# Kernel optimization log

Measured on AMD Instinct MI355X. Metric: run time of the kernel, lower is better.

## Reference

```python
import jax, jax.numpy as jnp
import numpy as np

N_LAYERS = 6
N_HEADS = 16
D_MODEL = 1024
D_HEAD = D_MODEL // N_HEADS
D_FF = 4096
VOCAB = 32000
MAX_LEN = 1024
B, T = 2, 1024
NEG = -1e9
EPS = 1e-5


def layernorm(x, s, b):
    mu = jnp.mean(x, axis=-1, keepdims=True)
    var = jnp.mean(jnp.square(x - mu), axis=-1, keepdims=True)
    return (x - mu) * jax.lax.rsqrt(var + EPS) * s + b


def setup_inputs() -> dict:
    key = jax.random.key(0)
    ks = jax.random.split(key, 8)
    s = 0.02
    return {
        "idx": jax.random.randint(ks[0], (B, T), 0, VOCAB),
        "tok_emb": jax.random.normal(ks[1], (VOCAB, D_MODEL), jnp.float32) * s,
        "pos_emb": jax.random.normal(ks[2], (MAX_LEN, D_MODEL), jnp.float32) * s,
        "ln1_s": jnp.ones((N_LAYERS, D_MODEL), jnp.float32),
        "ln1_b": jnp.zeros((N_LAYERS, D_MODEL), jnp.float32),
        "qkv_w": jax.random.normal(ks[3], (N_LAYERS, D_MODEL, 3 * D_MODEL), jnp.float32) * s,
        "qkv_b": jnp.zeros((N_LAYERS, 3 * D_MODEL), jnp.float32),
        "out_w": jax.random.normal(ks[4], (N_LAYERS, D_MODEL, D_MODEL), jnp.float32) * s,
        "out_b": jnp.zeros((N_LAYERS, D_MODEL), jnp.float32),
        "ln2_s": jnp.ones((N_LAYERS, D_MODEL), jnp.float32),
        "ln2_b": jnp.zeros((N_LAYERS, D_MODEL), jnp.float32),
        "mlp_w1": jax.random.normal(ks[5], (N_LAYERS, D_MODEL, D_FF), jnp.float32) * s,
        "mlp_b1": jnp.zeros((N_LAYERS, D_FF), jnp.float32),
        "mlp_w2": jax.random.normal(ks[6], (N_LAYERS, D_FF, D_MODEL), jnp.float32) * s,
        "mlp_b2": jnp.zeros((N_LAYERS, D_MODEL), jnp.float32),
        "lnf_s": jnp.ones((D_MODEL,), jnp.float32),
        "lnf_b": jnp.zeros((D_MODEL,), jnp.float32),
        "head_w": jax.random.normal(ks[7], (D_MODEL, VOCAB), jnp.float32) * s,
    }


def reference(idx, tok_emb, pos_emb, ln1_s, ln1_b, qkv_w, qkv_b, out_w, out_b,
              ln2_s, ln2_b, mlp_w1, mlp_b1, mlp_w2, mlp_b2, lnf_s, lnf_b, head_w):
    b, t = idx.shape
    x = tok_emb[idx] + pos_emb[:t]  # [B,T,D]
    causal = jnp.tril(jnp.ones((t, t), dtype=bool))
    scale = 1.0 / np.sqrt(D_HEAD)
    for l in range(N_LAYERS):
        h = layernorm(x, ln1_s[l], ln1_b[l])
        qkv = h @ qkv_w[l] + qkv_b[l]  # [B,T,3D]
        q, k, v = jnp.split(qkv, 3, axis=-1)
        q = q.reshape(b, t, N_HEADS, D_HEAD).transpose(0, 2, 1, 3)
        k = k.reshape(b, t, N_HEADS, D_HEAD).transpose(0, 2, 1, 3)
        v = v.reshape(b, t, N_HEADS, D_HEAD).transpose(0, 2, 1, 3)
        att = jnp.einsum('bhqd,bhkd->bhqk', q, k) * scale
        att = jnp.where(causal, att, NEG)
        att = jax.nn.softmax(att, axis=-1)
        y = jnp.einsum('bhqk,bhkd->bhqd', att, v)
        y = y.transpose(0, 2, 1, 3).reshape(b, t, D_MODEL)
        x = x + (y @ out_w[l] + out_b[l])
        h = layernorm(x, ln2_s[l], ln2_b[l])
        m = jax.nn.gelu(h @ mlp_w1[l] + mlp_b1[l], approximate=False) @ mlp_w2[l] + mlp_b2[l]
        x = x + m
    x = layernorm(x, lnf_s, lnf_b)
    logits = x @ head_w  # [B,T,V]
    return logits
```

## Files before the change

kernel.cpp:

```cpp
#include <hip/hip_runtime.h>


#define T_SEQ 1024
#define NTOK  2048
#define DM    1024
#define DFF   4096
#define NH    16
#define DH    64
#define NL    6
#define VOCAB 32000

typedef short sx8 __attribute__((ext_vector_type(8)));
typedef float fx4 __attribute__((ext_vector_type(4)));
typedef unsigned short usx4 __attribute__((ext_vector_type(4)));
typedef unsigned int   uix4 __attribute__((ext_vector_type(4)));

__device__ __forceinline__ unsigned short f2bf(float f) {
  union { float f; unsigned u; } c; c.f = f;
  unsigned r = c.u + 0x7FFFu + ((c.u >> 16) & 1u);
  return (unsigned short)(r >> 16);
}
__device__ __forceinline__ float bf2f(unsigned short u) {
  union { unsigned u; float f; } c; c.u = ((unsigned)u) << 16;
  return c.f;
}

__device__ __forceinline__ void gload_lds16(const unsigned short* g, unsigned short* l) {
  __builtin_amdgcn_global_load_lds(
      (const __attribute__((address_space(1))) unsigned int*)g,
      (__attribute__((address_space(3))) unsigned int*)l, 16, 0, 0);
}

__device__ __forceinline__ int xcd_swizzle(int orig, int nwg) {
  int q = nwg >> 3, r = nwg & 7;
  int xcd = orig & 7, idx = orig >> 3;
  int base = (xcd < r) ? xcd * (q + 1) : r * (q + 1) + (xcd - r) * q;
  return base + idx;
}

__global__ __launch_bounds__(256) void k_embed(const int* __restrict__ idx,
                                               const float* __restrict__ tok,
                                               const float* __restrict__ pos,
                                               float* __restrict__ x) {
  int token = blockIdx.x;
  int t = token & (T_SEQ - 1);
  int id = idx[token];
  int c = threadIdx.x * 4;
  float4 tv = *(const float4*)&tok[(size_t)id * DM + c];
  float4 pv = *(const float4*)&pos[(size_t)t * DM + c];
  float4 r;
  r.x = tv.x + pv.x; r.y = tv.y + pv.y; r.z = tv.z + pv.z; r.w = tv.w + pv.w;
  *(float4*)&x[(size_t)token * DM + c] = r;
}

__global__ __launch_bounds__(256) void k_ln(const float* __restrict__ x,
                                            const float* __restrict__ g,
                                            const float* __restrict__ b,
                                            unsigned short* __restrict__ h) {
  int row = blockIdx.x;
  int tid = threadIdx.x;
  float4 v = *(const float4*)&x[(size_t)row * DM + tid * 4];
  float s = v.x + v.y + v.z + v.w;
  float q = v.x * v.x + v.y * v.y + v.z * v.z + v.w * v.w;
  for (int off = 32; off > 0; off >>= 1) {
    s += __shfl_down(s, off);
    q += __shfl_down(q, off);
  }
  __shared__ float red[8];
  int wid = tid >> 6, lane = tid & 63;
  if (lane == 0) { red[wid] = s; red[4 + wid] = q; }
  __syncthreads();
  s = red[0] + red[1] + red[2] + red[3];
  q = red[4] + red[5] + red[6] + red[7];
  float mu = s * (1.0f / DM);
  float var = q * (1.0f / DM) - mu * mu;
  float rstd = rsqrtf(var + 1e-5f);
  float4 gg = *(const float4*)&g[tid * 4];
  float4 bb = *(const float4*)&b[tid * 4];
  usx4 o;
  o[0] = f2bf((v.x - mu) * rstd * gg.x + bb.x);
  o[1] = f2bf((v.y - mu) * rstd * gg.y + bb.y);
  o[2] = f2bf((v.z - mu) * rstd * gg.z + bb.z);
  o[3] = f2bf((v.w - mu) * rstd * gg.w + bb.w);
  *(usx4*)&h[(size_t)row * DM + tid * 4] = o;
}

__global__ __launch_bounds__(256) void k_reduce_ln(const unsigned short* __restrict__ part,
                                                   float* __restrict__ x,
                                                   const float* __restrict__ g,
                                                   const float* __restrict__ b,
                                                   unsigned short* __restrict__ h) {
  int row = blockIdx.x;
  int tid = threadIdx.x;
  int c = tid * 4;
  float4 v = *(const float4*)&x[(size_t)row * DM + c];
#pragma unroll
  for (int s4 = 0; s4 < 4; ++s4) {
    usx4 p = *(const usx4*)&part[((size_t)s4 * NTOK + row) * DM + c];
    v.x += bf2f(p[0]); v.y += bf2f(p[1]); v.z += bf2f(p[2]); v.w += bf2f(p[3]);
  }
  *(float4*)&x[(size_t)row * DM + c] = v;
  float s = v.x + v.y + v.z + v.w;
  float q = v.x * v.x + v.y * v.y + v.z * v.z + v.w * v.w;
  for (int off = 32; off > 0; off >>= 1) {
    s += __shfl_down(s, off);
    q += __shfl_down(q, off);
  }
  __shared__ float red[8];
  int wid = tid >> 6, lane = tid & 63;
  if (lane == 0) { red[wid] = s; red[4 + wid] = q; }
  __syncthreads();
  s = red[0] + red[1] + red[2] + red[3];
  q = red[4] + red[5] + red[6] + red[7];
  float mu = s * (1.0f / DM);
  float var = q * (1.0f / DM) - mu * mu;
  float rstd = rsqrtf(var + 1e-5f);
  float4 gg = *(const float4*)&g[c];
  float4 bb = *(const float4*)&b[c];
  usx4 o;
  o[0] = f2bf((v.x - mu) * rstd * gg.x + bb.x);
  o[1] = f2bf((v.y - mu) * rstd * gg.y + bb.y);
  o[2] = f2bf((v.z - mu) * rstd * gg.z + bb.z);
  o[3] = f2bf((v.w - mu) * rstd * gg.w + bb.w);
  *(usx4*)&h[(size_t)row * DM + c] = o;
}

__global__ __launch_bounds__(256) void k_wtrans(const float* __restrict__ W,
                                                unsigned short* __restrict__ WT,
                                                int K, int N) {
  __shared__ float t[64][68];
  int k0 = blockIdx.x * 64, n0 = blockIdx.y * 64;
  int tid = threadIdx.x;
#pragma unroll
  for (int i = 0; i < 4; ++i) {
    int chunk = i * 256 + tid;
    int r = chunk >> 4, c = (chunk & 15) << 2;
    float4 v = *(const float4*)&W[(size_t)(k0 + r) * N + n0 + c];
    t[r][c] = v.x; t[r][c + 1] = v.y; t[r][c + 2] = v.z; t[r][c + 3] = v.w;
  }
  __syncthreads();
#pragma unroll
  for (int i = 0; i < 4; ++i) {
    int chunk = i * 256 + tid;
    int n = chunk >> 4, c = (chunk & 15) << 2;
    usx4 o;
    o[0] = f2bf(t[c][n]);
    o[1] = f2bf(t[c + 1][n]);
    o[2] = f2bf(t[c + 2][n]);
    o[3] = f2bf(t[c + 3][n]);
    *(usx4*)&WT[(size_t)(n0 + n) * K + k0 + c] = o;
  }
}

template <int EPI>
__global__ __launch_bounds__(256) void k_gemm(const unsigned short* __restrict__ A,
                                              const unsigned short* __restrict__ BT,
                                              const float* __restrict__ bias,
                                              unsigned short* __restrict__ part,
                                              unsigned short* __restrict__ outb,
                                              float* __restrict__ outf,
                                              int N, int K, int NT, int KS) {
  __shared__ unsigned short As[2][128 * 64];
  __shared__ unsigned short Bs[2][128 * 64];
  int tid = threadIdx.x;
  int wid = tid >> 6, lane = tid & 63;
  int lr = lane & 15, lg = lane >> 4;

  int id = xcd_swizzle(blockIdx.x, gridDim.x);
  int mt = id & 15;
  int rest = id >> 4;
  int nt = rest % NT;
  int ks = rest / NT;
  int m0 = mt * 128, n0 = nt * 128;
  int Kslice = K / KS;
  int kbeg = ks * Kslice;
  int nk = Kslice >> 6;

  int wm = (wid >> 1) * 64, wn = (wid & 1) * 64;

  fx4 acc[4][4] = {};

#define GSTAGE(buf, kt)                                                         \
  {                                                                             \
    _Pragma("unroll")                                                           \
    for (int i = 0; i < 4; ++i) {                                               \
      int chunk = i * 256 + tid;                                                \
      int r = chunk >> 3, slot = chunk & 7;                                     \
      int c = ((slot ^ (r & 7)) << 3);                                          \
      gload_lds16(&A[(size_t)(m0 + r) * K + (kt) + c], &As[buf][chunk << 3]);   \
      gload_lds16(&BT[(size_t)(n0 + r) * K + (kt) + c], &Bs[buf][chunk << 3]);  \
    }                                                                           \
  }

  GSTAGE(0, kbeg);
  for (int ik = 0; ik < nk; ++ik) {
    int cur = ik & 1;
    if (ik + 1 < nk) {
      GSTAGE(cur ^ 1, kbeg + (ik + 1) * 64);
      asm volatile("s_waitcnt vmcnt(8)" ::: "memory");
    } else {
      asm volatile("s_waitcnt vmcnt(0)" ::: "memory");
    }
    __builtin_amdgcn_sched_barrier(0);
    __builtin_amdgcn_s_barrier();
    __builtin_amdgcn_sched_barrier(0);
#pragma unroll
    for (int kk = 0; kk < 2; ++kk) {
      int slotz = (kk * 4 + lg) ^ (lr & 7);
      sx8 fa[4], fb[4];
#pragma unroll
      for (int mi = 0; mi < 4; ++mi)
        fa[mi] = *(const sx8*)&As[cur][(wm + mi * 16 + lr) * 64 + slotz * 8];
#pragma unroll
      for (int ni = 0; ni < 4; ++ni)
        fb[ni] = *(const sx8*)&Bs[cur][(wn + ni * 16 + lr) * 64 + slotz * 8];
#pragma unroll
      for (int mi = 0; mi < 4; ++mi)
#pragma unroll
        for (int ni = 0; ni < 4; ++ni)
          acc[mi][ni] = __builtin_amdgcn_mfma_f32_16x16x32_bf16(fb[ni], fa[mi], acc[mi][ni], 0, 0, 0);
    }
    asm volatile("s_waitcnt lgkmcnt(0)" ::: "memory");
    __builtin_amdgcn_sched_barrier(0);
    __builtin_amdgcn_s_barrier();
  }
#undef GSTAGE

#pragma unroll
  for (int ni = 0; ni < 4; ++ni) {
    int col0 = n0 + wn + ni * 16 + lg * 4;
    float4 bv = {0.f, 0.f, 0.f, 0.f};
    if (bias && ks == 0) bv = *(const float4*)&bias[col0];
#pragma unroll
    for (int mi = 0; mi < 4; ++mi) {
      int row = m0 + wm + mi * 16 + lr;
      float v0 = acc[mi][ni][0] + bv.x;
      float v1 = acc[mi][ni][1] + bv.y;
      float v2 = acc[mi][ni][2] + bv.z;
      float v3 = acc[mi][ni][3] + bv.w;
      if constexpr (EPI == 0) {
        int bb = row >> 10, tt = row & 1023;
        if (col0 < 2048) {
          int which = col0 >> 10;
          int hc = col0 & 1023;
          usx4 o = {f2bf(v0), f2bf(v1), f2bf(v2), f2bf(v3)};
          *(usx4*)&outb[(size_t)which * NTOK * DM +
                        (((size_t)bb * NH + (hc >> 6)) * T_SEQ + tt) * DH + (hc & 63)] = o;
        } else {
          int dc = col0 - 2048;
          unsigned short* vt = outb + (size_t)2 * NTOK * DM;
          size_t base = (((size_t)bb * NH + (dc >> 6)) * DH + (dc & 63)) * T_SEQ + tt;
          vt[base] = f2bf(v0);
          vt[base + T_SEQ] = f2bf(v1);
          vt[base + 2 * T_SEQ] = f2bf(v2);
          vt[base + 3 * T_SEQ] = f2bf(v3);
        }
      } else if constexpr (EPI == 1) {
        usx4 o;
        o[0] = f2bf(0.5f * v0 * (1.0f + erff(v0 * 0.70710678f)));
        o[1] = f2bf(0.5f * v1 * (1.0f + erff(v1 * 0.70710678f)));
        o[2] = f2bf(0.5f * v2 * (1.0f + erff(v2 * 0.70710678f)));
        o[3] = f2bf(0.5f * v3 * (1.0f + erff(v3 * 0.70710678f)));
        *(usx4*)&outb[(size_t)row * N + col0] = o;
      } else {
        usx4 o = {f2bf(v0), f2bf(v1), f2bf(v2), f2bf(v3)};
        *(usx4*)&part[((size_t)ks * NTOK + row) * DM + col0] = o;
      }
    }
  }
}

#define LDSUB(buf, ab, kk) (lds + (((buf) * 2 + (ab)) * 2 + (kk)) * 8192)

__device__ __forceinline__ void stage_half(const unsigned short* g, int rowstride,
                                           unsigned short* ldsbase, int tid, int k0) {
#pragma unroll
  for (int r = 0; r < 2; ++r) {
    int chunk = r * 512 + tid;
    int row = chunk >> 2, slot = chunk & 3;
    gload_lds16(g + (size_t)row * rowstride + k0 + ((slot ^ ((row >> 1) & 3)) << 3),
                ldsbase + (chunk << 3));
  }
}

__global__ __launch_bounds__(512, 2) void k_gemm256(const unsigned short* __restrict__ A,
                                                    const unsigned short* __restrict__ BT,
                                                    float* __restrict__ outf,
                                                    int N, int K) {
  __shared__ unsigned short lds[8 * 8192];
  int tid = threadIdx.x;
  int wid = tid >> 6, lane = tid & 63;
  int lr = lane & 15, lg = lane >> 4;
  int wm2 = wid >> 2, wn4 = wid & 3;
  int id = xcd_swizzle(blockIdx.x, gridDim.x);
  int mt = id & 7, nt = id >> 3;
  int m0 = mt * 256, n0 = nt * 256;
  const unsigned short* Ab = A + (size_t)m0 * K;
  const unsigned short* Bb = BT + (size_t)n0 * K;
  int NIT = K >> 7;
  int swz = (lg ^ ((lr >> 1) & 3)) << 3;
  float* obase = outf + (size_t)(m0 + wm2 * 128 + lr) * N + n0 + wn4 * 64 + lg * 4;

  fx4 acc[8][4] = {};

  stage_half(Ab, K, LDSUB(0, 0, 0), tid, 0);
  stage_half(Bb, K, LDSUB(0, 1, 0), tid, 0);
  stage_half(Ab, K, LDSUB(0, 0, 1), tid, 32);
  stage_half(Bb, K, LDSUB(0, 1, 1), tid, 32);
  stage_half(Ab, K, LDSUB(1, 0, 0), tid, 64);
  stage_half(Bb, K, LDSUB(1, 1, 0), tid, 64);
  stage_half(Ab, K, LDSUB(1, 0, 1), tid, 96);
  asm volatile("s_waitcnt vmcnt(6)" ::: "memory");
  __builtin_amdgcn_s_barrier();

#define PHASE(BUF, KK, NHH, LOADA, STG, VMW)                                         \
  {                                                                                  \
    if (LOADA) {                                                                     \
      const unsigned short* sA = LDSUB(BUF, 0, KK);                                  \
      _Pragma("unroll")                                                              \
      for (int mi = 0; mi < 8; ++mi)                                                 \
        fa[mi] = *(const sx8*)&sA[(wm2 * 128 + mi * 16 + lr) * 32 + swz];            \
    }                                                                                \
    {                                                                                \
      const unsigned short* sB = LDSUB(BUF, 1, KK);                                  \
      _Pragma("unroll")                                                              \
      for (int j = 0; j < 2; ++j)                                                    \
        fb[j] = *(const sx8*)&sB[(wn4 * 64 + (NHH) * 32 + j * 16 + lr) * 32 + swz];  \
    }                                                                                \
    STG;                                                                             \
    VMW;                                                                             \
    __builtin_amdgcn_sched_barrier(0);                                               \
    __builtin_amdgcn_s_barrier();                                                    \
    asm volatile("s_waitcnt lgkmcnt(0)" ::: "memory");                               \
    __builtin_amdgcn_sched_barrier(0);                                               \
    __builtin_amdgcn_s_setprio(1);                                                   \
    _Pragma("unroll")                                                                \
    for (int mi = 0; mi < 8; ++mi) {                                                 \
      acc[mi][(NHH) * 2 + 0] = __builtin_amdgcn_mfma_f32_16x16x32_bf16(              \
          fb[0], fa[mi], acc[mi][(NHH) * 2 + 0], 0, 0, 0);                           \
      acc[mi][(NHH) * 2 + 1] = __builtin_amdgcn_mfma_f32_16x16x32_bf16(              \
          fb[1], fa[mi], acc[mi][(NHH) * 2 + 1], 0, 0, 0);                           \
    }                                                                                \
    __builtin_amdgcn_s_setprio(0);                                                   \
    __builtin_amdgcn_sched_barrier(0);                                               \
    __builtin_amdgcn_s_barrier();                                                    \
  }

  for (int it = 0; it < NIT; ++it) {
    bool st = (it < NIT - 1);
    bool last = (it == NIT - 1);
    int t1k = (2 * it + 1) * 64;
    int t2k = (2 * it + 2) * 64;
    int t3k = (2 * it + 3) * 64;
    sx8 fa[8], fb[2];

    PHASE(0, 0, 0, true,
          { stage_half(Bb, K, LDSUB(1, 1, 1), tid, t1k + 32); }, {});
    PHASE(0, 0, 1, false,
          { if (st) stage_half(Ab, K, LDSUB(0, 0, 0), tid, t2k); }, {});
    PHASE(0, 1, 0, true,
          { if (st) stage_half(Bb, K, LDSUB(0, 1, 0), tid, t2k); }, {});
    PHASE(0, 1, 1, false,
          { if (st) stage_half(Ab, K, LDSUB(0, 0, 1), tid, t2k + 32); },
          { if (last) { asm volatile("s_waitcnt vmcnt(0)" ::: "memory"); }
            else      { asm volatile("s_waitcnt vmcnt(6)" ::: "memory"); } });
    PHASE(1, 0, 0, true,
          { if (st) stage_half(Bb, K, LDSUB(0, 1, 1), tid, t2k + 32); }, {});
    PHASE(1, 0, 1, false,
          { if (st) stage_half(Ab, K, LDSUB(1, 0, 0), tid, t3k); }, {});
    PHASE(1, 1, 0, true,
          { if (st) stage_half(Bb, K, LDSUB(1, 1, 0), tid, t3k); }, {});
    if (last) {
#pragma unroll
      for (int mi = 0; mi < 8; ++mi) {
        *(float4*)(obase + (size_t)mi * 16 * N) =
            (float4){acc[mi][0][0], acc[mi][0][1], acc[mi][0][2], acc[mi][0][3]};
        *(float4*)(obase + (size_t)mi * 16 * N + 16) =
            (float4){acc[mi][1][0], acc[mi][1][1], acc[mi][1][2], acc[mi][1][3]};
      }
    }
    PHASE(1, 1, 1, false,
          { if (st) stage_half(Ab, K, LDSUB(1, 0, 1), tid, t3k + 32); },
          { if (!last) { asm volatile("s_waitcnt vmcnt(6)" ::: "memory"); } });
  }
#undef PHASE

#pragma unroll
  for (int mi = 0; mi < 8; ++mi) {
    *(float4*)(obase + (size_t)mi * 16 * N + 32) =
        (float4){acc[mi][2][0], acc[mi][2][1], acc[mi][2][2], acc[mi][2][3]};
    *(float4*)(obase + (size_t)mi * 16 * N + 48) =
        (float4){acc[mi][3][0], acc[mi][3][1], acc[mi][3][2], acc[mi][3][3]};
  }
}

__global__ __launch_bounds__(256) void k_attn(const unsigned short* __restrict__ gq,
                                              const unsigned short* __restrict__ gk,
                                              const unsigned short* __restrict__ gvt,
                                              unsigned short* __restrict__ y) {
  __shared__ unsigned short Ks[128 * 64];
  __shared__ unsigned short Vt[64 * 128];
  __shared__ unsigned short Pw[4][16 * 136];
  int id = xcd_swizzle(blockIdx.x, gridDim.x);
  int bh = id >> 4, qt = 15 - (id & 15);
  int tid = threadIdx.x, wid = tid >> 6, lane = tid & 63;
  int lr = lane & 15, lg = lane >> 4;
  int q0 = qt * 64 + wid * 16;
  int qg = q0 + lr;
  const float SCL = 0.125f * 1.44269504f;

  sx8 qf[2];
  {
    const unsigned short* qp = gq + ((size_t)bh * T_SEQ + qg) * DH + lg * 8;
    qf[0] = *(const sx8*)qp;
    qf[1] = *(const sx8*)(qp + 32);
  }

  fx4 yacc[4] = {};
  float mrun = -1e30f, lrun = 0.f;

  int jmax = qt >> 1;
  for (int j = 0; j <= jmax; ++j) {
    int kt0 = j * 128;
    __syncthreads();
#pragma unroll
    for (int i = 0; i < 4; ++i) {
      int chunk = i * 256 + tid;
      {
        int r = chunk >> 3, s = chunk & 7;
        gload_lds16(&gk[((size_t)bh * T_SEQ + kt0 + r) * DH + ((s ^ (r & 7)) << 3)],
                    &Ks[chunk << 3]);
      }
      {
        int r = chunk >> 4, s = chunk & 15;
        gload_lds16(&gvt[((size_t)bh * DH + r) * T_SEQ + kt0 + ((s ^ (r & 15)) << 3)],
                    &Vt[chunk << 3]);
      }
    }
    __syncthreads();

    fx4 st[8] = {};
#pragma unroll
    for (int kk = 0; kk < 2; ++kk) {
      int slotz = (kk * 4 + lg) ^ (lr & 7);
#pragma unroll
      for (int mi = 0; mi < 8; ++mi) {
        sx8 kb = *(const sx8*)&Ks[(mi * 16 + lr) * 64 + slotz * 8];
        st[mi] = __builtin_amdgcn_mfma_f32_16x16x32_bf16(kb, qf[kk], st[mi], 0, 0, 0);
      }
    }

    float pvv[8][4];
    float pmax = -1e30f;
    bool lastj = (j == jmax);
#pragma unroll
    for (int mi = 0; mi < 8; ++mi)
#pragma unroll
      for (int rg = 0; rg < 4; ++rg) {
        float val = st[mi][rg] * SCL;
        if (lastj && (kt0 + mi * 16 + lg * 4 + rg) > qg) val = -1e30f;
        pvv[mi][rg] = val;
        pmax = fmaxf(pmax, val);
      }
    pmax = fmaxf(pmax, __shfl_xor(pmax, 16));
    pmax = fmaxf(pmax, __shfl_xor(pmax, 32));
    if (!__all(pmax <= mrun + 11.5f)) {
      float mnew = fmaxf(mrun, pmax);
      float sc = exp2f(mrun - mnew);
      lrun *= sc;
#pragma unroll
      for (int dt = 0; dt < 4; ++dt)
#pragma unroll
        for (int rg = 0; rg < 4; ++rg) yacc[dt][rg] *= sc;
      mrun = mnew;
    }
    float ps = 0.f;
#pragma unroll
    for (int mi = 0; mi < 8; ++mi)
#pragma unroll
      for (int rg = 0; rg < 4; ++rg) {
        float e = exp2f(pvv[mi][rg] - mrun);
        pvv[mi][rg] = e;
        ps += e;
      }
    ps += __shfl_xor(ps, 16);
    ps += __shfl_xor(ps, 32);
    lrun += ps;

#pragma unroll
    for (int mi = 0; mi < 8; ++mi)
#pragma unroll
      for (int rp = 0; rp < 2; ++rp) {
        unsigned pk = (unsigned)f2bf(pvv[mi][rp * 2]) |
                      ((unsigned)f2bf(pvv[mi][rp * 2 + 1]) << 16);
        *(unsigned*)&Pw[wid][lr * 136 + mi * 16 + lg * 4 + rp * 2] = pk;
      }

#pragma unroll
    for (int kk = 0; kk < 4; ++kk) {
      sx8 pa = *(const sx8*)&Pw[wid][lr * 136 + kk * 32 + lg * 8];
      int slotz = (kk * 4 + lg) ^ lr;
#pragma unroll
      for (int dt = 0; dt < 4; ++dt) {
        sx8 vb = *(const sx8*)&Vt[(dt * 16 + lr) * 128 + slotz * 8];
        yacc[dt] = __builtin_amdgcn_mfma_f32_16x16x32_bf16(vb, pa, yacc[dt], 0, 0, 0);
      }
    }
  }

  float inv = 1.0f / lrun;
  int tok = (bh >> 4) * T_SEQ + qg;
  int colbase = (bh & 15) * DH;
#pragma unroll
  for (int dt = 0; dt < 4; ++dt) {
    usx4 o;
#pragma unroll
    for (int rg = 0; rg < 4; ++rg) o[rg] = f2bf(yacc[dt][rg] * inv);
    *(usx4*)&y[(size_t)tok * DM + colbase + dt * 16 + lg * 4] = o;
  }
}

extern "C" void kernel_launch(void* const* d_in, const int* in_sizes, int n_in,
                              void* d_out, int out_size, void* d_ws, size_t ws_size,
                              hipStream_t stream) {
  (void)in_sizes; (void)n_in; (void)out_size; (void)ws_size;
  const int*   idx     = (const int*)d_in[0];
  const float* tok_emb = (const float*)d_in[1];
  const float* pos_emb = (const float*)d_in[2];
  const float* ln1_s   = (const float*)d_in[3];
  const float* ln1_b   = (const float*)d_in[4];
  const float* qkv_w   = (const float*)d_in[5];
  const float* qkv_b   = (const float*)d_in[6];
  const float* out_w   = (const float*)d_in[7];
  const float* out_b   = (const float*)d_in[8];
  const float* ln2_s   = (const float*)d_in[9];
  const float* ln2_b   = (const float*)d_in[10];
  const float* mlp_w1  = (const float*)d_in[11];
  const float* mlp_b1  = (const float*)d_in[12];
  const float* mlp_w2  = (const float*)d_in[13];
  const float* mlp_b2  = (const float*)d_in[14];
  const float* lnf_s   = (const float*)d_in[15];
  const float* lnf_b   = (const float*)d_in[16];
  const float* head_w  = (const float*)d_in[17];

  char* p = (char*)d_ws;
  float* x          = (float*)p;          p += (size_t)NTOK * DM * 4;
  unsigned short* h = (unsigned short*)p; p += (size_t)NTOK * DM * 2;
  unsigned short* qkvb = (unsigned short*)p; p += (size_t)3 * NTOK * DM * 2;
  unsigned short* yb = (unsigned short*)p; p += (size_t)NTOK * DM * 2;
  unsigned short* m1 = (unsigned short*)p; p += (size_t)NTOK * DFF * 2;
  unsigned short* wt = (unsigned short*)p;
  unsigned short* part = (unsigned short*)(p + 32 * 1024 * 1024);

  dim3 blk(256);

  k_embed<<<NTOK, blk, 0, stream>>>(idx, tok_emb, pos_emb, x);
  k_ln<<<NTOK, blk, 0, stream>>>(x, ln1_s, ln1_b, h);

  for (int l = 0; l < NL; ++l) {
    k_wtrans<<<dim3(DM / 64, 3 * DM / 64), blk, 0, stream>>>(qkv_w + (size_t)l * DM * 3 * DM, wt, DM, 3 * DM);
    k_gemm<0><<<16 * 24, blk, 0, stream>>>(h, wt, qkv_b + l * 3 * DM,
                                           nullptr, qkvb, nullptr, 3 * DM, DM, 24, 1);
    k_attn<<<512, blk, 0, stream>>>(qkvb, qkvb + (size_t)NTOK * DM,
                                    qkvb + (size_t)2 * NTOK * DM, yb);
    k_wtrans<<<dim3(DM / 64, DM / 64), blk, 0, stream>>>(out_w + (size_t)l * DM * DM, wt, DM, DM);
    k_gemm<2><<<16 * 8 * 4, blk, 0, stream>>>(yb, wt, out_b + l * DM,
                                              part, nullptr, nullptr, DM, DM, 8, 4);
    k_reduce_ln<<<NTOK, blk, 0, stream>>>(part, x, ln2_s + l * DM, ln2_b + l * DM, h);
    k_wtrans<<<dim3(DM / 64, DFF / 64), blk, 0, stream>>>(mlp_w1 + (size_t)l * DM * DFF, wt, DM, DFF);
    k_gemm<1><<<16 * 32, blk, 0, stream>>>(h, wt, mlp_b1 + l * DFF,
                                           nullptr, m1, nullptr, DFF, DM, 32, 1);
    k_wtrans<<<dim3(DFF / 64, DM / 64), blk, 0, stream>>>(mlp_w2 + (size_t)l * DFF * DM, wt, DFF, DM);
    k_gemm<2><<<16 * 8 * 4, blk, 0, stream>>>(m1, wt, mlp_b2 + l * DM,
                                              part, nullptr, nullptr, DM, DFF, 8, 4);
    if (l < NL - 1)
      k_reduce_ln<<<NTOK, blk, 0, stream>>>(part, x, ln1_s + (l + 1) * DM, ln1_b + (l + 1) * DM, h);
    else
      k_reduce_ln<<<NTOK, blk, 0, stream>>>(part, x, lnf_s, lnf_b, h);
  }

  k_wtrans<<<dim3(DM / 64, VOCAB / 64), blk, 0, stream>>>(head_w, wt, DM, VOCAB);
  k_gemm256<<<1000, 512, 0, stream>>>(h, wt, (float*)d_out, VOCAB, DM);
}
```

Before: 1.160 ms.

## Batch per-layer weight transposes, fuse embed+LN, use packed bf16 conversions

Combines the four per-layer weight transpose launches into one larger launch that writes into separate buffers, and fuses the embedding with the first layernorm. Replaces the software bf16 rounding with the hardware v_cvt_pk_bf16_f32 instruction across all epilogues. Splits the attention causal-mask loop so only the diagonal tile evaluates the mask. The aim is fewer launches, better occupancy for the transpose, and cheaper conversion arithmetic, at the cost of needing more workspace for the transposed weights, which must not overlap the partial-sum buffer.

```diff
diff --git a/kernel.cpp b/kernel.cpp
--- a/kernel.cpp
+++ b/kernel.cpp
@@ -24,6 +24,11 @@
   union { unsigned u; float f; } c; c.u = ((unsigned)u) << 16;
   return c.f;
 }
+__device__ __forceinline__ unsigned cvt_pk_bf16(float lo, float hi) {
+  unsigned r;
+  asm("v_cvt_pk_bf16_f32 %0, %1, %2" : "=v"(r) : "v"(lo), "v"(hi));
+  return r;
+}
 
 __device__ __forceinline__ void gload_lds16(const unsigned short* g, unsigned short* l) {
   __builtin_amdgcn_global_load_lds(
@@ -38,68 +43,23 @@
   return base + idx;
 }
 
-__global__ __launch_bounds__(256) void k_embed(const int* __restrict__ idx,
-                                               const float* __restrict__ tok,
-                                               const float* __restrict__ pos,
-                                               float* __restrict__ x) {
+__global__ __launch_bounds__(256) void k_embed_ln(const int* __restrict__ idx,
+                                                  const float* __restrict__ tok,
+                                                  const float* __restrict__ pos,
+                                                  const float* __restrict__ g,
+                                                  const float* __restrict__ b,
+                                                  float* __restrict__ x,
+                                                  unsigned short* __restrict__ h) {
   int token = blockIdx.x;
   int t = token & (T_SEQ - 1);
   int id = idx[token];
-  int c = threadIdx.x * 4;
+  int tid = threadIdx.x;
+  int c = tid * 4;
   float4 tv = *(const float4*)&tok[(size_t)id * DM + c];
   float4 pv = *(const float4*)&pos[(size_t)t * DM + c];
-  float4 r;
-  r.x = tv.x + pv.x; r.y = tv.y + pv.y; r.z = tv.z + pv.z; r.w = tv.w + pv.w;
-  *(float4*)&x[(size_t)token * DM + c] = r;
-}
-
-__global__ __launch_bounds__(256) void k_ln(const float* __restrict__ x,
-                                            const float* __restrict__ g,
-                                            const float* __restrict__ b,
-                                            unsigned short* __restrict__ h) {
-  int row = blockIdx.x;
-  int tid = threadIdx.x;
-  float4 v = *(const float4*)&x[(size_t)row * DM + tid * 4];
-  float s = v.x + v.y + v.z + v.w;
-  float q = v.x * v.x + v.y * v.y + v.z * v.z + v.w * v.w;
-  for (int off = 32; off > 0; off >>= 1) {
-    s += __shfl_down(s, off);
-    q += __shfl_down(q, off);
-  }
-  __shared__ float red[8];
-  int wid = tid >> 6, lane = tid & 63;
-  if (lane == 0) { red[wid] = s; red[4 + wid] = q; }
-  __syncthreads();
-  s = red[0] + red[1] + red[2] + red[3];
-  q = red[4] + red[5] + red[6] + red[7];
-  float mu = s * (1.0f / DM);
-  float var = q * (1.0f / DM) - mu * mu;
-  float rstd = rsqrtf(var + 1e-5f);
-  float4 gg = *(const float4*)&g[tid * 4];
-  float4 bb = *(const float4*)&b[tid * 4];
-  usx4 o;
-  o[0] = f2bf((v.x - mu) * rstd * gg.x + bb.x);
-  o[1] = f2bf((v.y - mu) * rstd * gg.y + bb.y);
-  o[2] = f2bf((v.z - mu) * rstd * gg.z + bb.z);
-  o[3] = f2bf((v.w - mu) * rstd * gg.w + bb.w);
-  *(usx4*)&h[(size_t)row * DM + tid * 4] = o;
-}
-
-__global__ __launch_bounds__(256) void k_reduce_ln(const unsigned short* __restrict__ part,
-                                                   float* __restrict__ x,
-                                                   const float* __restrict__ g,
-                                                   const float* __restrict__ b,
-                                                   unsigned short* __restrict__ h) {
-  int row = blockIdx.x;
-  int tid = threadIdx.x;
-  int c = tid * 4;
-  float4 v = *(const float4*)&x[(size_t)row * DM + c];
-#pragma unroll
-  for (int s4 = 0; s4 < 4; ++s4) {
-    usx4 p = *(const usx4*)&part[((size_t)s4 * NTOK + row) * DM + c];
-    v.x += bf2f(p[0]); v.y += bf2f(p[1]); v.z += bf2f(p[2]); v.w += bf2f(p[3]);
-  }
-  *(float4*)&x[(size_t)row * DM + c] = v;
+  float4 v;
+  v.x = tv.x + pv.x; v.y = tv.y + pv.y; v.z = tv.z + pv.z; v.w = tv.w + pv.w;
+  *(float4*)&x[(size_t)token * DM + c] = v;
   float s = v.x + v.y + v.z + v.w;
   float q = v.x * v.x + v.y * v.y + v.z * v.z + v.w * v.w;
   for (int off = 32; off > 0; off >>= 1) {
@@ -117,20 +77,54 @@
   float rstd = rsqrtf(var + 1e-5f);
   float4 gg = *(const float4*)&g[c];
   float4 bb = *(const float4*)&b[c];
-  usx4 o;
-  o[0] = f2bf((v.x - mu) * rstd * gg.x + bb.x);
-  o[1] = f2bf((v.y - mu) * rstd * gg.y + bb.y);
-  o[2] = f2bf((v.z - mu) * rstd * gg.z + bb.z);
-  o[3] = f2bf((v.w - mu) * rstd * gg.w + bb.w);
-  *(usx4*)&h[(size_t)row * DM + c] = o;
-}
-
-__global__ __launch_bounds__(256) void k_wtrans(const float* __restrict__ W,
-                                                unsigned short* __restrict__ WT,
-                                                int K, int N) {
+  uint2 o;
+  o.x = cvt_pk_bf16((v.x - mu) * rstd * gg.x + bb.x, (v.y - mu) * rstd * gg.y + bb.y);
+  o.y = cvt_pk_bf16((v.z - mu) * rstd * gg.z + bb.z, (v.w - mu) * rstd * gg.w + bb.w);
+  *(uint2*)&h[(size_t)token * DM + c] = o;
+}
+
+__global__ __launch_bounds__(256) void k_reduce_ln(const unsigned short* __restrict__ part,
+                                                   float* __restrict__ x,
+                                                   const float* __restrict__ g,
+                                                   const float* __restrict__ b,
+                                                   unsigned short* __restrict__ h) {
+  int row = blockIdx.x;
+  int tid = threadIdx.x;
+  int c = tid * 4;
+  float4 v = *(const float4*)&x[(size_t)row * DM + c];
+#pragma unroll
+  for (int s4 = 0; s4 < 4; ++s4) {
+    usx4 p = *(const usx4*)&part[((size_t)s4 * NTOK + row) * DM + c];
+    v.x += bf2f(p[0]); v.y += bf2f(p[1]); v.z += bf2f(p[2]); v.w += bf2f(p[3]);
+  }
+  *(float4*)&x[(size_t)row * DM + c] = v;
+  float s = v.x + v.y + v.z + v.w;
+  float q = v.x * v.x + v.y * v.y + v.z * v.z + v.w * v.w;
+  for (int off = 32; off > 0; off >>= 1) {
+    s += __shfl_down(s, off);
+    q += __shfl_down(q, off);
+  }
+  __shared__ float red[8];
+  int wid = tid >> 6, lane = tid & 63;
+  if (lane == 0) { red[wid] = s; red[4 + wid] = q; }
+  __syncthreads();
+  s = red[0] + red[1] + red[2] + red[3];
+  q = red[4] + red[5] + red[6] + red[7];
+  float mu = s * (1.0f / DM);
+  float var = q * (1.0f / DM) - mu * mu;
+  float rstd = rsqrtf(var + 1e-5f);
+  float4 gg = *(const float4*)&g[c];
+  float4 bb = *(const float4*)&b[c];
+  uint2 o;
+  o.x = cvt_pk_bf16((v.x - mu) * rstd * gg.x + bb.x, (v.y - mu) * rstd * gg.y + bb.y);
+  o.y = cvt_pk_bf16((v.z - mu) * rstd * gg.z + bb.z, (v.w - mu) * rstd * gg.w + bb.w);
+  *(uint2*)&h[(size_t)row * DM + c] = o;
+}
+
+__device__ __forceinline__ void wtrans_body(const float* __restrict__ W,
+                                            unsigned short* __restrict__ WT,
+                                            int K, int N, int k0, int n0, int tid) {
   __shared__ float t[64][68];
-  int k0 = blockIdx.x * 64, n0 = blockIdx.y * 64;
-  int tid = threadIdx.x;
 #pragma unroll
   for (int i = 0; i < 4; ++i) {
     int chunk = i * 256 + tid;
@@ -143,13 +137,35 @@
   for (int i = 0; i < 4; ++i) {
     int chunk = i * 256 + tid;
     int n = chunk >> 4, c = (chunk & 15) << 2;
-    usx4 o;
-    o[0] = f2bf(t[c][n]);
-    o[1] = f2bf(t[c + 1][n]);
-    o[2] = f2bf(t[c + 2][n]);
-    o[3] = f2bf(t[c + 3][n]);
-    *(usx4*)&WT[(size_t)(n0 + n) * K + k0 + c] = o;
-  }
+    uint2 o;
+    o.x = cvt_pk_bf16(t[c][n], t[c + 1][n]);
+    o.y = cvt_pk_bf16(t[c + 2][n], t[c + 3][n]);
+    *(uint2*)&WT[(size_t)(n0 + n) * K + k0 + c] = o;
+  }
+}
+
+__global__ __launch_bounds__(256) void k_wtrans(const float* __restrict__ W,
+                                                unsigned short* __restrict__ WT,
+                                                int K, int N) {
+  wtrans_body(W, WT, K, N, blockIdx.x * 64, blockIdx.y * 64, threadIdx.x);
+}
+
+__global__ __launch_bounds__(256) void k_wtrans4(const float* __restrict__ W0,
+                                                 const float* __restrict__ W1,
+                                                 const float* __restrict__ W2,
+                                                 const float* __restrict__ W3,
+                                                 unsigned short* __restrict__ T0,
+                                                 unsigned short* __restrict__ T1,
+                                                 unsigned short* __restrict__ T2,
+                                                 unsigned short* __restrict__ T3) {
+  int id = blockIdx.x;
+  const float* W; unsigned short* WT; int K, N, lid;
+  if (id < 768)       { W = W0; WT = T0; K = 1024; N = 3072; lid = id; }
+  else if (id < 1024) { W = W1; WT = T1; K = 1024; N = 1024; lid = id - 768; }
+  else if (id < 2048) { W = W2; WT = T2; K = 1024; N = 4096; lid = id - 1024; }
+  else                { W = W3; WT = T3; K = 4096; N = 1024; lid = id - 2048; }
+  int kb = K >> 6;
+  wtrans_body(W, WT, K, N, (lid % kb) * 64, (lid / kb) * 64, threadIdx.x);
 }
 
 template <int EPI>
@@ -243,9 +259,9 @@
         if (col0 < 2048) {
           int which = col0 >> 10;
           int hc = col0 & 1023;
-          usx4 o = {f2bf(v0), f2bf(v1), f2bf(v2), f2bf(v3)};
-          *(usx4*)&outb[(size_t)which * NTOK * DM +
-                        (((size_t)bb * NH + (hc >> 6)) * T_SEQ + tt) * DH + (hc & 63)] = o;
+          uint2 o = {cvt_pk_bf16(v0, v1), cvt_pk_bf16(v2, v3)};
+          *(uint2*)&outb[(size_t)which * NTOK * DM +
+                         (((size_t)bb * NH + (hc >> 6)) * T_SEQ + tt) * DH + (hc & 63)] = o;
         } else {
           int dc = col0 - 2048;
           unsigned short* vt = outb + (size_t)2 * NTOK * DM;
@@ -256,15 +272,15 @@
           vt[base + 3 * T_SEQ] = f2bf(v3);
         }
       } else if constexpr (EPI == 1) {
-        usx4 o;
-        o[0] = f2bf(0.5f * v0 * (1.0f + erff(v0 * 0.70710678f)));
-        o[1] = f2bf(0.5f * v1 * (1.0f + erff(v1 * 0.70710678f)));
-        o[2] = f2bf(0.5f * v2 * (1.0f + erff(v2 * 0.70710678f)));
-        o[3] = f2bf(0.5f * v3 * (1.0f + erff(v3 * 0.70710678f)));
-        *(usx4*)&outb[(size_t)row * N + col0] = o;
+        float g0 = 0.5f * v0 * (1.0f + erff(v0 * 0.70710678f));
+        float g1 = 0.5f * v1 * (1.0f + erff(v1 * 0.70710678f));
+        float g2 = 0.5f * v2 * (1.0f + erff(v2 * 0.70710678f));
+        float g3 = 0.5f * v3 * (1.0f + erff(v3 * 0.70710678f));
+        uint2 o = {cvt_pk_bf16(g0, g1), cvt_pk_bf16(g2, g3)};
+        *(uint2*)&outb[(size_t)row * N + col0] = o;
       } else {
-        usx4 o = {f2bf(v0), f2bf(v1), f2bf(v2), f2bf(v3)};
-        *(usx4*)&part[((size_t)ks * NTOK + row) * DM + col0] = o;
+        uint2 o = {cvt_pk_bf16(v0, v1), cvt_pk_bf16(v2, v3)};
+        *(uint2*)&part[((size_t)ks * NTOK + row) * DM + col0] = o;
       }
     }
   }
@@ -452,16 +468,26 @@
 
     float pvv[8][4];
     float pmax = -1e30f;
-    bool lastj = (j == jmax);
-#pragma unroll
-    for (int mi = 0; mi < 8; ++mi)
-#pragma unroll
-      for (int rg = 0; rg < 4; ++rg) {
-        float val = st[mi][rg] * SCL;
-        if (lastj && (kt0 + mi * 16 + lg * 4 + rg) > qg) val = -1e30f;
-        pvv[mi][rg] = val;
-        pmax = fmaxf(pmax, val);
-      }
+    if (j < jmax) {
+#pragma unroll
+      for (int mi = 0; mi < 8; ++mi)
+#pragma unroll
+        for (int rg = 0; rg < 4; ++rg) {
+          float val = st[mi][rg] * SCL;
+          pvv[mi][rg] = val;
+          pmax = fmaxf(pmax, val);
+        }
+    } else {
+#pragma unroll
+      for (int mi = 0; mi < 8; ++mi)
+#pragma unroll
+        for (int rg = 0; rg < 4; ++rg) {
+          float val = st[mi][rg] * SCL;
+          if ((kt0 + mi * 16 + lg * 4 + rg) > qg) val = -1e30f;
+          pvv[mi][rg] = val;
+          pmax = fmaxf(pmax, val);
+        }
+    }
     pmax = fmaxf(pmax, __shfl_xor(pmax, 16));
     pmax = fmaxf(pmax, __shfl_xor(pmax, 32));
     if (!__all(pmax <= mrun + 11.5f)) {
@@ -491,8 +517,7 @@
     for (int mi = 0; mi < 8; ++mi)
 #pragma unroll
       for (int rp = 0; rp < 2; ++rp) {
-        unsigned pk = (unsigned)f2bf(pvv[mi][rp * 2]) |
-                      ((unsigned)f2bf(pvv[mi][rp * 2 + 1]) << 16);
+        unsigned pk = cvt_pk_bf16(pvv[mi][rp * 2], pvv[mi][rp * 2 + 1]);
         *(unsigned*)&Pw[wid][lr * 136 + mi * 16 + lg * 4 + rp * 2] = pk;
       }
 
@@ -513,10 +538,10 @@
   int colbase = (bh & 15) * DH;
 #pragma unroll
   for (int dt = 0; dt < 4; ++dt) {
-    usx4 o;
-#pragma unroll
-    for (int rg = 0; rg < 4; ++rg) o[rg] = f2bf(yacc[dt][rg] * inv);
-    *(usx4*)&y[(size_t)tok * DM + colbase + dt * 16 + lg * 4] = o;
+    uint2 o;
+    o.x = cvt_pk_bf16(yacc[dt][0] * inv, yacc[dt][1] * inv);
+    o.y = cvt_pk_bf16(yacc[dt][2] * inv, yacc[dt][3] * inv);
+    *(uint2*)&y[(size_t)tok * DM + colbase + dt * 16 + lg * 4] = o;
   }
 }
 
@@ -550,28 +575,32 @@
   unsigned short* yb = (unsigned short*)p; p += (size_t)NTOK * DM * 2;
   unsigned short* m1 = (unsigned short*)p; p += (size_t)NTOK * DFF * 2;
   unsigned short* wt = (unsigned short*)p;
+  unsigned short* wtq  = wt;
+  unsigned short* wto  = wt + (size_t)3 * 1024 * 1024;
+  unsigned short* wtm1 = wt + (size_t)4 * 1024 * 1024;
+  unsigned short* wtm2 = wt + (size_t)8 * 1024 * 1024;
   unsigned short* part = (unsigned short*)(p + 32 * 1024 * 1024);
 
   dim3 blk(256);
 
-  k_embed<<<NTOK, blk, 0, stream>>>(idx, tok_emb, pos_emb, x);
-  k_ln<<<NTOK, blk, 0, stream>>>(x, ln1_s, ln1_b, h);
+  k_embed_ln<<<NTOK, blk, 0, stream>>>(idx, tok_emb, pos_emb, ln1_s, ln1_b, x, h);
 
   for (int l = 0; l < NL; ++l) {
-    k_wtrans<<<dim3(DM / 64, 3 * DM / 64), blk, 0, stream>>>(qkv_w + (size_t)l * DM * 3 * DM, wt, DM, 3 * DM);
-    k_gemm<0><<<16 * 24, blk, 0, stream>>>(h, wt, qkv_b + l * 3 * DM,
+    k_wtrans4<<<3072, blk, 0, stream>>>(qkv_w + (size_t)l * DM * 3 * DM,
+                                        out_w + (size_t)l * DM * DM,
+                                        mlp_w1 + (size_t)l * DM * DFF,
+                                        mlp_w2 + (size_t)l * DFF * DM,
+                                        wtq, wto, wtm1, wtm2);
+    k_gemm<0><<<16 * 24, blk, 0, stream>>>(h, wtq, qkv_b + l * 3 * DM,
                                            nullptr, qkvb, nullptr, 3 * DM, DM, 24, 1);
     k_attn<<<512, blk, 0, stream>>>(qkvb, qkvb + (size_t)NTOK * DM,
                                     qkvb + (size_t)2 * NTOK * DM, yb);
-    k_wtrans<<<dim3(DM / 64, DM / 64), blk, 0, stream>>>(out_w + (size_t)l * DM * DM, wt, DM, DM);
-    k_gemm<2><<<16 * 8 * 4, blk, 0, stream>>>(yb, wt, out_b + l * DM,
+    k_gemm<2><<<16 * 8 * 4, blk, 0, stream>>>(yb, wto, out_b + l * DM,
                                               part, nullptr, nullptr, DM, DM, 8, 4);
     k_reduce_ln<<<NTOK, blk, 0, stream>>>(part, x, ln2_s + l * DM, ln2_b + l * DM, h);
-    k_wtrans<<<dim3(DM / 64, DFF / 64), blk, 0, stream>>>(mlp_w1 + (size_t)l * DM * DFF, wt, DM, DFF);
-    k_gemm<1><<<16 * 32, blk, 0, stream>>>(h, wt, mlp_b1 + l * DFF,
+    k_gemm<1><<<16 * 32, blk, 0, stream>>>(h, wtm1, mlp_b1 + l * DFF,
                                            nullptr, m1, nullptr, DFF, DM, 32, 1);
-    k_wtrans<<<dim3(DFF / 64, DM / 64), blk, 0, stream>>>(mlp_w2 + (size_t)l * DFF * DM, wt, DFF, DM);
-    k_gemm<2><<<16 * 8 * 4, blk, 0, stream>>>(m1, wt, mlp_b2 + l * DM,
+    k_gemm<2><<<16 * 8 * 4, blk, 0, stream>>>(m1, wtm2, mlp_b2 + l * DM,
                                               part, nullptr, nullptr, DM, DFF, 8, 4);
     if (l < NL - 1)
       k_reduce_ln<<<NTOK, blk, 0, stream>>>(part, x, ln1_s + (l + 1) * DM, ln1_b + (l + 1) * DM, h);
```

New measurement: 1.090 ms. 6.0% less time.
